# Kernel tuning notes

Hardware: AMD Instinct MI355X
Metric: run time of the kernel (lower is better)

## Reference

```python
import jax, jax.numpy as jnp
import numpy as np

L_LAYERS = 3
N_EGO = 1024
N_EDGE = 49152
M_MODES = 6
HID = 256
N_HEADS = 8
LN_EPS = 1e-5


def _layernorm(x, w, b):
    mu = jnp.mean(x, axis=-1, keepdims=True)
    var = jnp.var(x, axis=-1, keepdims=True)
    return (x - mu) * jax.lax.rsqrt(var + LN_EPS) * w + b


def setup_inputs() -> dict:
    key = jax.random.key(0)
    ks = jax.random.split(key, 16)
    f32 = jnp.float32
    H, Hh, L = HID, HID // 2, L_LAYERS

    def p(k, shape, s=0.02):
        return jax.random.normal(k, shape, f32) * s

    inp = {
        "batch": jnp.sort(jax.random.randint(ks[0], (N_EDGE,), 0, N_EGO)),
        "ego_feature": jax.random.normal(ks[1], (N_EGO, M_MODES, H), f32),
        "edge_feat": jax.random.normal(ks[2], (N_EDGE, M_MODES, Hh), f32),
        "node_feat": jax.random.normal(ks[3], (N_EDGE, M_MODES, Hh), f32),
        # stacked per-layer params
        "Wk": p(ks[4], (L, Hh, H)), "bk": jnp.zeros((L, H), f32),
        "Wq": p(ks[5], (L, H, H)), "bq": jnp.zeros((L, H), f32),
        "Wv1": p(ks[6], (L, Hh, H)), "bv1": jnp.zeros((L, H), f32),
        "Wv2": p(ks[7], (L, Hh, H)), "bv2": jnp.zeros((L, H), f32),
        "ln1_w": jnp.ones((L, H), f32), "ln1_b": jnp.zeros((L, H), f32),
        "ln2_w": jnp.ones((L, H), f32), "ln2_b": jnp.zeros((L, H), f32),
        "W1": p(ks[8], (L, H, H)), "b1": jnp.zeros((L, H), f32),
        "W2": p(ks[9], (L, H, H)), "b2": jnp.zeros((L, H), f32),
        "Wd": p(ks[10], (L, H, H)), "bd": jnp.zeros((L, H), f32),
    }
    return inp


def reference(batch, ego_feature, edge_feat, node_feat,
              Wk, bk, Wq, bq, Wv1, bv1, Wv2, bv2,
              ln1_w, ln1_b, ln2_w, ln2_b, W1, b1, W2, b2, Wd, bd):
    N, M, H = ego_feature.shape
    E = edge_feat.shape[0]
    h = N_HEADS
    dh = H // h
    L = Wk.shape[0]

    ego = ego_feature
    for i in range(L):
        # --- self-attention block (edge gather -> segment softmax -> scatter sum) ---
        xn = _layernorm(ego, ln1_w[i], ln1_b[i])                 # [N,M,H]
        k = (edge_feat @ Wk[i] + bk[i]).reshape(E, M, h, dh)     # [E,M,h,dh]
        q = (xn @ Wq[i] + bq[i]).reshape(N, M, h, dh)            # [N,M,h,dh]
        v = (edge_feat @ Wv1[i] + bv1[i]
             + node_feat @ Wv2[i] + bv2[i]).reshape(E, M, h, dh)
        scores = jnp.sum(k * q[batch], axis=-1)                  # [E,M,h]
        # segment softmax over edges grouped by ego index
        mx = jax.ops.segment_max(scores, batch, num_segments=N)  # [N,M,h]
        e = jnp.exp(scores - mx[batch])
        denom = jax.ops.segment_sum(e, batch, num_segments=N)
        alpha = e / (denom[batch] + 1e-16)                       # [E,M,h]
        agg = jax.ops.segment_sum((v * alpha[..., None]).reshape(E, M, H),
                                  batch, num_segments=N)         # [N,M,H]
        ego = ego + agg
        # --- ff block (note: 'dropout' in the original is actually a Linear) ---
        yn = _layernorm(ego, ln2_w[i], ln2_b[i])
        hmid = jax.nn.relu(yn @ W1[i] + b1[i])
        hmid = hmid @ Wd[i] + bd[i]
        ego = ego + (hmid @ W2[i] + b2[i])
    return ego
```

## Files before the change

### kernel.cpp

```cpp
#include <hip/hip_runtime.h>
#include <hip/hip_bf16.h>

#define L_LAYERS 3
#define N_EGO    1024
#define N_EDGE   49152
#define M_MODES  6
#define HID      256
#define HH       128
#define NH       8
#define DH       32
#define LN_EPS   1e-5f
#define ESS      (M_MODES * 129)
#define TE       8
#define FR       8

using bf16 = __hip_bfloat16;

__device__ __forceinline__ float cvt(float x) { return x; }
__device__ __forceinline__ float cvt(bf16 x)  { return __bfloat162float(x); }
__device__ __forceinline__ float b2f(unsigned s) {
    union { float f; unsigned u; } x; x.u = s << 16; return x.f;
}

template <typename T>
__device__ __forceinline__ float ldv(const void* p, size_t i) {
    return cvt(((const T*)p)[i]);
}

__device__ __forceinline__ float block_sum256(float v, float* buf) {
    int t = threadIdx.x;
    buf[t] = v;
    __syncthreads();
    #pragma unroll
    for (int s = 128; s > 0; s >>= 1) {
        if (t < s) buf[t] += buf[t + s];
        __syncthreads();
    }
    float r = buf[0];
    __syncthreads();
    return r;
}

__global__ void offsets_kernel(const int* __restrict__ batch, int* __restrict__ offs,
                               const void* __restrict__ ln1w, int* __restrict__ flag) {
    int n = blockIdx.x * blockDim.x + threadIdx.x;
    if (n == 0) {
        const unsigned short* u = (const unsigned short*)ln1w;
        flag[0] = (u[0] == 0x3F80 && u[1] == 0x3F80) ? 0 : 1;
    }
    if (n > N_EGO) return;
    int lo = 0, hi = N_EDGE;
    while (lo < hi) {
        int mid = (lo + hi) >> 1;
        if (batch[mid] < n) lo = mid + 1; else hi = mid;
    }
    offs[n] = lo;
}

template <typename T>
__device__ void init_body(const void* src, float* dst) {
    int i = blockIdx.x * 256 + threadIdx.x;
    dst[i] = ldv<T>(src, i);
}
__global__ void init_kernel(const void* __restrict__ src, float* __restrict__ dst,
                            const int* __restrict__ flag) {
    if (flag[0]) init_body<float>(src, dst); else init_body<bf16>(src, dst);
}

template <typename T>
__device__ void wkt_body(const void* Wk, float* WkT) {
    int idx = blockIdx.x * 256 + threadIdx.x;
    int l   = idx / (HH * HID);
    int rem = idx - l * (HH * HID);
    int j   = rem >> 8;
    int cc  = rem & (HID - 1);
    WkT[(size_t)l * HID * HH + (size_t)cc * HH + j] = ldv<T>(Wk, idx);
}
__global__ void wkt_kernel(const void* __restrict__ Wk, float* __restrict__ WkT,
                           const int* __restrict__ flag) {
    if (flag[0]) wkt_body<float>(Wk, WkT); else wkt_body<bf16>(Wk, WkT);
}

template <typename T>
__device__ void prep_body(const float* ego, const float* WkT, const void* bk,
                          const void* Wq, const void* bq, const void* lnw,
                          const void* lnb, int layer,
                          bf16* qk, float* qb) {
    extern __shared__ float sm[];
    float* xn_s = sm;
    float* q_s  = sm + 1536;
    float* sbuf = sm + 3072;
    int n = blockIdx.x, c = threadIdx.x;
    size_t vo = (size_t)layer * HID;

    float lw = ldv<T>(lnw, vo + c), lb = ldv<T>(lnb, vo + c);
    for (int m = 0; m < M_MODES; m++) {
        float x  = ego[((size_t)n * M_MODES + m) * HID + c];
        float mu = block_sum256(x, sbuf) * (1.0f / HID);
        float d  = x - mu;
        float var = block_sum256(d * d, sbuf) * (1.0f / HID);
        xn_s[m * HID + c] = d * rsqrtf(var + LN_EPS) * lw + lb;
    }
    __syncthreads();

    {
        size_t wo = (size_t)layer * HID * HID;
        float acc[M_MODES];
        float bqv = ldv<T>(bq, vo + c);
        #pragma unroll
        for (int m = 0; m < M_MODES; m++) acc[m] = bqv;
        for (int k = 0; k < HID; k++) {
            float w = ldv<T>(Wq, wo + (size_t)k * HID + c);
            #pragma unroll
            for (int m = 0; m < M_MODES; m++) acc[m] += xn_s[m * HID + k] * w;
        }
        #pragma unroll
        for (int m = 0; m < M_MODES; m++) q_s[m * HID + c] = acc[m];
    }
    __syncthreads();

    {
        const float* WT = WkT + (size_t)layer * HID * HH;
        int j = c & (HH - 1), hg = c >> 7;
        #pragma unroll
        for (int hh = 0; hh < NH / 2; hh++) {
            int h = hg * (NH / 2) + hh;
            float a[M_MODES];
            #pragma unroll
            for (int m = 0; m < M_MODES; m++) a[m] = 0.f;
            for (int u = 0; u < DH; u++) {
                float w = WT[(size_t)(h * DH + u) * HH + j];
                #pragma unroll
                for (int m = 0; m < M_MODES; m++)
                    a[m] += q_s[m * HID + h * DH + u] * w;
            }
            #pragma unroll
            for (int m = 0; m < M_MODES; m++)
                qk[((size_t)n * 48 + m * NH + h) * HH + j] = __float2bfloat16(a[m]);
        }
        if (c < M_MODES * NH) {
            int m = c >> 3, h = c & 7;
            float s = 0.f;
            for (int u = 0; u < DH; u++)
                s += ldv<T>(bk, vo + h * DH + u) * q_s[m * HID + h * DH + u];
            qb[n * 48 + c] = s;
        }
    }
}
__global__ void prep_kernel(const float* __restrict__ ego, const float* __restrict__ WkT,
                            const void* __restrict__ bk, const void* __restrict__ Wq,
                            const void* __restrict__ bq, const void* __restrict__ lnw,
                            const void* __restrict__ lnb, int layer,
                            bf16* __restrict__ qk, float* __restrict__ qb,
                            const int* __restrict__ flag) {
    if (flag[0]) prep_body<float>(ego, WkT, bk, Wq, bq, lnw, lnb, layer, qk, qb);
    else         prep_body<bf16 >(ego, WkT, bk, Wq, bq, lnw, lnb, layer, qk, qb);
}

template <typename T>
__device__ void score_body(const void* ef, const bf16* qk, const float* qb,
                           const int* batch, bf16* scores) {
    extern __shared__ float es[];
    int c = threadIdx.x;
    int e0 = blockIdx.x * TE;

    if constexpr (sizeof(T) == 2) {
        const uint4* src = (const uint4*)((const char*)ef + (size_t)e0 * (M_MODES * HH) * 2);
        #pragma unroll
        for (int it = 0; it < 3; it++) {
            int v = it * 256 + c;
            uint4 u = src[v];
            int eo = v / 96, r = v - eo * 96, m = r >> 4, j = (r & 15) * 8;
            float* d = es + eo * ESS + m * 129 + j;
            d[0] = b2f(u.x & 0xffffu); d[1] = b2f(u.x >> 16);
            d[2] = b2f(u.y & 0xffffu); d[3] = b2f(u.y >> 16);
            d[4] = b2f(u.z & 0xffffu); d[5] = b2f(u.z >> 16);
            d[6] = b2f(u.w & 0xffffu); d[7] = b2f(u.w >> 16);
        }
    } else {
        const float4* src = (const float4*)((const char*)ef + (size_t)e0 * (M_MODES * HH) * 4);
        #pragma unroll
        for (int it = 0; it < 6; it++) {
            int v = it * 256 + c;
            float4 u = src[v];
            int eo = v / 192, r = v - eo * 192, m = r >> 5, j = (r & 31) * 4;
            float* d = es + eo * ESS + m * 129 + j;
            d[0] = u.x; d[1] = u.y; d[2] = u.z; d[3] = u.w;
        }
    }
    __syncthreads();

    int g = c & 63, w = c >> 6;
    if (g < M_MODES * NH) {
        #pragma unroll
        for (int sub = 0; sub < TE / 4; sub++) {
            int eo = sub * 4 + w, e = e0 + eo;
            int b = batch[e];
            const uint4* qrow = (const uint4*)(qk + ((size_t)b * 48 + g) * HH);
            const float* ep = es + eo * ESS + (g >> 3) * 129;
            float acc = qb[b * 48 + g];
            #pragma unroll
            for (int v = 0; v < 16; v++) {
                uint4 u = qrow[v];
                const float* e8 = ep + v * 8;
                acc += e8[0] * b2f(u.x & 0xffffu) + e8[1] * b2f(u.x >> 16)
                     + e8[2] * b2f(u.y & 0xffffu) + e8[3] * b2f(u.y >> 16)
                     + e8[4] * b2f(u.z & 0xffffu) + e8[5] * b2f(u.z >> 16)
                     + e8[6] * b2f(u.w & 0xffffu) + e8[7] * b2f(u.w >> 16);
            }
            scores[(size_t)e * 48 + g] = __float2bfloat16(acc);
        }
    }
}
__global__ void score_kernel(const void* __restrict__ ef, const bf16* __restrict__ qk,
                             const float* __restrict__ qb, const int* __restrict__ batch,
                             bf16* __restrict__ scores, const int* __restrict__ flag) {
    if (flag[0]) score_body<float>(ef, qk, qb, batch, scores);
    else         score_body<bf16 >(ef, qk, qb, batch, scores);
}

__global__ void softmax_kernel(bf16* __restrict__ scores, const int* __restrict__ offs) {
    __shared__ float red[4][48];
    int n = blockIdx.x;
    int s0 = offs[n], t1 = offs[n + 1];
    if (s0 >= t1) return;
    int c = threadIdx.x, g = c & 63, w = c >> 6;
    bool act = g < M_MODES * NH;
    float mx = -INFINITY;
    if (act) {
        for (int e = s0 + w; e < t1; e += 4)
            mx = fmaxf(mx, cvt(scores[(size_t)e * 48 + g]));
        red[w][g] = mx;
    }
    __syncthreads();
    if (act) {
        mx = fmaxf(fmaxf(red[0][g], red[1][g]), fmaxf(red[2][g], red[3][g]));
        if (!(mx == mx)) mx = 0.f;
    }
    __syncthreads();
    float den = 0.f;
    if (act) {
        for (int e = s0 + w; e < t1; e += 4) {
            float v = expf(fminf(cvt(scores[(size_t)e * 48 + g]) - mx, 0.f));
            scores[(size_t)e * 48 + g] = __float2bfloat16(v);
            den += v;
        }
        red[w][g] = den;
    }
    __syncthreads();
    if (act) {
        den = red[0][g] + red[1][g] + red[2][g] + red[3][g];
        float inv = 1.0f / (den + 1e-16f);
        for (int e = s0 + w; e < t1; e += 4)
            scores[(size_t)e * 48 + g] =
                __float2bfloat16(cvt(scores[(size_t)e * 48 + g]) * inv);
    }
}

template <typename T>
__device__ void agg_body(const void* ef, const void* nf,
                         const void* Wv1, const void* bv1,
                         const void* Wv2, const void* bv2, int layer,
                         const bf16* alpha, const int* offs, float* ego) {
    extern __shared__ float sm[];
    float* A    = sm;
    float* alf  = sm + 12288;
    float* Ssum = alf + 768;
    int n = blockIdx.x, c = threadIdx.x;
    int s0 = offs[n], t1 = offs[n + 1];
    if (s0 >= t1) return;
    size_t vo = (size_t)layer * HID;
    int part = c >> 7, j = c & (HH - 1);
    const void* src = part ? nf : ef;

    float acc[48];
    #pragma unroll
    for (int i = 0; i < 48; i++) acc[i] = 0.f;
    float sa = 0.f;

    for (int e0 = s0; e0 < t1; e0 += 16) {
        int cnt = t1 - e0; if (cnt > 16) cnt = 16;
        __syncthreads();
        for (int idx = c; idx < cnt * 48; idx += 256)
            alf[idx] = cvt(alpha[(size_t)e0 * 48 + idx]);
        __syncthreads();
        for (int ee = 0; ee < cnt; ee++) {
            size_t ebase = (size_t)(e0 + ee) * (M_MODES * HH) + j;
            const float4* ap = (const float4*)(alf + ee * 48);
            #pragma unroll
            for (int m = 0; m < M_MODES; m++) {
                float val = ldv<T>(src, ebase + m * HH);
                float4 a0 = ap[m * 2 + 0];
                float4 a1 = ap[m * 2 + 1];
                acc[m*8+0] += a0.x * val; acc[m*8+1] += a0.y * val;
                acc[m*8+2] += a0.z * val; acc[m*8+3] += a0.w * val;
                acc[m*8+4] += a1.x * val; acc[m*8+5] += a1.y * val;
                acc[m*8+6] += a1.z * val; acc[m*8+7] += a1.w * val;
            }
        }
        if (c < 48)
            for (int ee = 0; ee < cnt; ee++) sa += alf[ee * 48 + c];
    }
    #pragma unroll
    for (int i = 0; i < 48; i++) A[(part * 48 + i) * HH + j] = acc[i];
    if (c < 48) Ssum[c] = sa;
    __syncthreads();

    size_t wo = (size_t)layer * HH * HID;
    int h = c >> 5;
    float bsum = ldv<T>(bv1, vo + c) + ldv<T>(bv2, vo + c);
    float out[M_MODES];
    #pragma unroll
    for (int m = 0; m < M_MODES; m++) out[m] = bsum * Ssum[m * NH + h];
    for (int jj = 0; jj < HH; jj++) {
        float w1 = ldv<T>(Wv1, wo + (size_t)jj * HID + c);
        float w2 = ldv<T>(Wv2, wo + (size_t)jj * HID + c);
        #pragma unroll
        for (int m = 0; m < M_MODES; m++)
            out[m] += A[(m * NH + h) * HH + jj] * w1
                    + A[(48 + m * NH + h) * HH + jj] * w2;
    }
    #pragma unroll
    for (int m = 0; m < M_MODES; m++)
        ego[((size_t)n * M_MODES + m) * HID + c] += out[m];
}
__global__ void agg_kernel(const void* __restrict__ ef, const void* __restrict__ nf,
                           const void* __restrict__ Wv1, const void* __restrict__ bv1,
                           const void* __restrict__ Wv2, const void* __restrict__ bv2,
                           int layer, const bf16* __restrict__ alpha,
                           const int* __restrict__ offs, float* __restrict__ ego,
                           const int* __restrict__ flag) {
    if (flag[0]) agg_body<float>(ef, nf, Wv1, bv1, Wv2, bv2, layer, alpha, offs, ego);
    else         agg_body<bf16 >(ef, nf, Wv1, bv1, Wv2, bv2, layer, alpha, offs, ego);
}

template <typename T>
__device__ void ffn_body(float* ego, const void* lnw, const void* lnb,
                         const void* W1, const void* b1, const void* Wd, const void* bd,
                         const void* W2, const void* b2, int layer) {
    extern __shared__ float sm[];
    float* xs  = sm;
    float* hs  = sm + 2048;
    float* sb1 = sm + 4096;
    float* sb2 = sm + 4352;
    int r0 = blockIdx.x * FR, c = threadIdx.x;
    size_t wo = (size_t)layer * HID * HID, vo = (size_t)layer * HID;
    float lw = ldv<T>(lnw, vo + c), lb = ldv<T>(lnb, vo + c);
    float x0[FR];
    for (int r = 0; r < FR; r++) {
        float x = ego[(size_t)(r0 + r) * HID + c];
        x0[r] = x;
        sb1[c] = x; sb2[c] = x * x;
        __syncthreads();
        for (int st = 128; st > 0; st >>= 1) {
            if (c < st) { sb1[c] += sb1[c + st]; sb2[c] += sb2[c + st]; }
            __syncthreads();
        }
        float mu  = sb1[0] * (1.0f / HID);
        float var = sb2[0] * (1.0f / HID) - mu * mu;
        __syncthreads();
        xs[r * HID + c] = (x - mu) * rsqrtf(fmaxf(var, 0.f) + LN_EPS) * lw + lb;
    }
    __syncthreads();
    float acc[FR];
    {
        float b = ldv<T>(b1, vo + c);
        #pragma unroll
        for (int r = 0; r < FR; r++) acc[r] = b;
        for (int k = 0; k < HID; k++) {
            float w = ldv<T>(W1, wo + (size_t)k * HID + c);
            #pragma unroll
            for (int r = 0; r < FR; r++) acc[r] += xs[r * HID + k] * w;
        }
        #pragma unroll
        for (int r = 0; r < FR; r++) hs[r * HID + c] = fmaxf(acc[r], 0.f);
    }
    __syncthreads();
    {
        float b = ldv<T>(bd, vo + c);
        #pragma unroll
        for (int r = 0; r < FR; r++) acc[r] = b;
        for (int k = 0; k < HID; k++) {
            float w = ldv<T>(Wd, wo + (size_t)k * HID + c);
            #pragma unroll
            for (int r = 0; r < FR; r++) acc[r] += hs[r * HID + k] * w;
        }
        __syncthreads();
        #pragma unroll
        for (int r = 0; r < FR; r++) xs[r * HID + c] = acc[r];
    }
    __syncthreads();
    {
        float b = ldv<T>(b2, vo + c);
        #pragma unroll
        for (int r = 0; r < FR; r++) acc[r] = b;
        for (int k = 0; k < HID; k++) {
            float w = ldv<T>(W2, wo + (size_t)k * HID + c);
            #pragma unroll
            for (int r = 0; r < FR; r++) acc[r] += xs[r * HID + k] * w;
        }
        #pragma unroll
        for (int r = 0; r < FR; r++)
            ego[(size_t)(r0 + r) * HID + c] = x0[r] + acc[r];
    }
}
__global__ void ffn_kernel(float* __restrict__ ego, const void* __restrict__ lnw,
                           const void* __restrict__ lnb, const void* __restrict__ W1,
                           const void* __restrict__ b1, const void* __restrict__ Wd,
                           const void* __restrict__ bd, const void* __restrict__ W2,
                           const void* __restrict__ b2, int layer,
                           const int* __restrict__ flag) {
    if (flag[0]) ffn_body<float>(ego, lnw, lnb, W1, b1, Wd, bd, W2, b2, layer);
    else         ffn_body<bf16 >(ego, lnw, lnb, W1, b1, Wd, bd, W2, b2, layer);
}

__global__ void out_kernel(const float* __restrict__ src, void* __restrict__ dst,
                           const int* __restrict__ flag) {
    int i = blockIdx.x * 256 + threadIdx.x;
    float v = src[i];
    if (flag[0]) ((float*)dst)[i] = v;
    else         ((bf16*)dst)[i] = __float2bfloat16(v);
}

extern "C" void kernel_launch(void* const* d_in, const int* in_sizes, int n_in,
                              void* d_out, int out_size, void* d_ws, size_t ws_size,
                              hipStream_t stream) {
    const int*  batch = (const int*)d_in[0];
    const void* ego_f = d_in[1];
    const void* edgef = d_in[2];
    const void* nodef = d_in[3];
    const void* Wk  = d_in[4];  const void* bk  = d_in[5];
    const void* Wq  = d_in[6];  const void* bq  = d_in[7];
    const void* Wv1 = d_in[8];  const void* bv1 = d_in[9];
    const void* Wv2 = d_in[10]; const void* bv2 = d_in[11];
    const void* ln1w = d_in[12]; const void* ln1b = d_in[13];
    const void* ln2w = d_in[14]; const void* ln2b = d_in[15];
    const void* W1  = d_in[16]; const void* b1  = d_in[17];
    const void* W2  = d_in[18]; const void* b2  = d_in[19];
    const void* Wd  = d_in[20]; const void* bd  = d_in[21];

    const size_t NMH = (size_t)N_EGO * M_MODES * HID;
    char* ws = (char*)d_ws;
    int*   flag   = (int*)ws;
    int*   offs   = flag + 1;
    float* ego_ws = (float*)(ws + 8192);
    bf16*  scores = (bf16*)(ws + 6299648);
    float* WkT    = (float*)(ws + 11018240);
    bf16*  qk_ws  = (bf16*)(ws + 11411456);
    float* qb_ws  = (float*)(ws + 23994368);

    const int ROWS = N_EGO * M_MODES;

    hipLaunchKernelGGL(offsets_kernel, dim3(5), dim3(256), 0, stream,
                       batch, offs, ln1w, flag);
    hipLaunchKernelGGL(init_kernel, dim3(ROWS), dim3(256), 0, stream,
                       ego_f, ego_ws, flag);
    hipLaunchKernelGGL(wkt_kernel, dim3(L_LAYERS * HH * HID / 256), dim3(256), 0, stream,
                       Wk, WkT, flag);

    const size_t PREP_LDS  = 3328 * 4;
    const size_t SCORE_LDS = (size_t)TE * ESS * 4;
    const size_t AGG_LDS   = (12288 + 768 + 48) * 4;
    const size_t FFN_LDS   = 4608 * 4;

    for (int i = 0; i < L_LAYERS; i++) {
        hipLaunchKernelGGL(prep_kernel, dim3(N_EGO), dim3(256), PREP_LDS, stream,
                           ego_ws, WkT, bk, Wq, bq, ln1w, ln1b, i, qk_ws, qb_ws, flag);
        hipLaunchKernelGGL(score_kernel, dim3(N_EDGE / TE), dim3(256), SCORE_LDS, stream,
                           edgef, qk_ws, qb_ws, batch, scores, flag);
        hipLaunchKernelGGL(softmax_kernel, dim3(N_EGO), dim3(256), 0, stream,
                           scores, offs);
        hipLaunchKernelGGL(agg_kernel, dim3(N_EGO), dim3(256), AGG_LDS, stream,
                           edgef, nodef, Wv1, bv1, Wv2, bv2, i, scores, offs,
                           ego_ws, flag);
        hipLaunchKernelGGL(ffn_kernel, dim3(ROWS / FR), dim3(256), FFN_LDS, stream,
                           ego_ws, ln2w, ln2b, W1, b1, Wd, bd, W2, b2, i, flag);
    }

    hipLaunchKernelGGL(out_kernel, dim3(ROWS), dim3(256), 0, stream,
                       ego_ws, d_out, flag);
}
```

Baseline: 1.321 ms.

## Split aggregation across edge/node parts, vectorize GEMV weight loads, use shuffle reductions

The aggregation kernel now runs on a 2D grid, with one block per ego for edge features and one for node features. Each block stages its feature tile in LDS, uses a padded accumulator layout, and merges results into ego with atomic adds. The prep and FFN matvecs switch from one column per thread to 8 contiguous columns per thread using 16-byte weight loads. LayerNorm reductions use wave shuffles that compute sum and sum-of-squares together, replacing the tree of block barriers. The variance formula changes to E[x^2]-mu^2, and the atomics make the summation order nondeterministic.

```diff
diff --git a/kernel.cpp b/kernel.cpp
--- a/kernel.cpp
+++ b/kernel.cpp
@@ -13,6 +13,7 @@
 #define ESS      (M_MODES * 129)
 #define TE       8
 #define FR       8
+#define AST      129
 
 using bf16 = __hip_bfloat16;
 
@@ -27,18 +28,37 @@
     return cvt(((const T*)p)[i]);
 }
 
-__device__ __forceinline__ float block_sum256(float v, float* buf) {
-    int t = threadIdx.x;
-    buf[t] = v;
-    __syncthreads();
+template <typename T>
+__device__ __forceinline__ void ld8(const void* p, size_t i, float* o);
+template <>
+__device__ __forceinline__ void ld8<bf16>(const void* p, size_t i, float* o) {
+    uint4 u = *(const uint4*)((const bf16*)p + i);
+    o[0] = b2f(u.x & 0xffffu); o[1] = b2f(u.x >> 16);
+    o[2] = b2f(u.y & 0xffffu); o[3] = b2f(u.y >> 16);
+    o[4] = b2f(u.z & 0xffffu); o[5] = b2f(u.z >> 16);
+    o[6] = b2f(u.w & 0xffffu); o[7] = b2f(u.w >> 16);
+}
+template <>
+__device__ __forceinline__ void ld8<float>(const void* p, size_t i, float* o) {
+    const float4* q = (const float4*)((const float*)p + i);
+    float4 a = q[0], b = q[1];
+    o[0] = a.x; o[1] = a.y; o[2] = a.z; o[3] = a.w;
+    o[4] = b.x; o[5] = b.y; o[6] = b.z; o[7] = b.w;
+}
+
+__device__ __forceinline__ void blk_sum2(float a, float b, float* red,
+                                         float* oa, float* ob) {
     #pragma unroll
-    for (int s = 128; s > 0; s >>= 1) {
-        if (t < s) buf[t] += buf[t + s];
-        __syncthreads();
-    }
-    float r = buf[0];
-    __syncthreads();
-    return r;
+    for (int off = 32; off > 0; off >>= 1) {
+        a += __shfl_down(a, off);
+        b += __shfl_down(b, off);
+    }
+    int w = threadIdx.x >> 6;
+    if ((threadIdx.x & 63) == 0) { red[w * 2] = a; red[w * 2 + 1] = b; }
+    __syncthreads();
+    *oa = red[0] + red[2] + red[4] + red[6];
+    *ob = red[1] + red[3] + red[5] + red[7];
+    __syncthreads();
 }
 
 __global__ void offsets_kernel(const int* __restrict__ batch, int* __restrict__ offs,
@@ -89,33 +109,37 @@
     extern __shared__ float sm[];
     float* xn_s = sm;
     float* q_s  = sm + 1536;
-    float* sbuf = sm + 3072;
+    float* red  = sm + 3072;
     int n = blockIdx.x, c = threadIdx.x;
     size_t vo = (size_t)layer * HID;
 
     float lw = ldv<T>(lnw, vo + c), lb = ldv<T>(lnb, vo + c);
     for (int m = 0; m < M_MODES; m++) {
-        float x  = ego[((size_t)n * M_MODES + m) * HID + c];
-        float mu = block_sum256(x, sbuf) * (1.0f / HID);
-        float d  = x - mu;
-        float var = block_sum256(d * d, sbuf) * (1.0f / HID);
-        xn_s[m * HID + c] = d * rsqrtf(var + LN_EPS) * lw + lb;
+        float x = ego[((size_t)n * M_MODES + m) * HID + c];
+        float s1, s2;
+        blk_sum2(x, x * x, red, &s1, &s2);
+        float mu  = s1 * (1.0f / HID);
+        float var = s2 * (1.0f / HID) - mu * mu;
+        xn_s[m * HID + c] = (x - mu) * rsqrtf(fmaxf(var, 0.f) + LN_EPS) * lw + lb;
     }
     __syncthreads();
 
     {
         size_t wo = (size_t)layer * HID * HID;
-        float acc[M_MODES];
-        float bqv = ldv<T>(bq, vo + c);
-        #pragma unroll
-        for (int m = 0; m < M_MODES; m++) acc[m] = bqv;
-        for (int k = 0; k < HID; k++) {
-            float w = ldv<T>(Wq, wo + (size_t)k * HID + c);
-            #pragma unroll
-            for (int m = 0; m < M_MODES; m++) acc[m] += xn_s[m * HID + k] * w;
-        }
-        #pragma unroll
-        for (int m = 0; m < M_MODES; m++) q_s[m * HID + c] = acc[m];
+        int co = (c & 31) * 8, mg = c >> 5;
+        if (mg < M_MODES) {
+            float acc[8], wv[8];
+            ld8<T>(bq, vo + co, acc);
+            #pragma unroll 4
+            for (int k = 0; k < HID; k++) {
+                ld8<T>(Wq, wo + (size_t)k * HID + co, wv);
+                float x = xn_s[mg * HID + k];
+                #pragma unroll
+                for (int i = 0; i < 8; i++) acc[i] += x * wv[i];
+            }
+            #pragma unroll
+            for (int i = 0; i < 8; i++) q_s[mg * HID + co + i] = acc[i];
+        }
     }
     __syncthreads();
 
@@ -262,67 +286,79 @@
                          const void* Wv1, const void* bv1,
                          const void* Wv2, const void* bv2, int layer,
                          const bf16* alpha, const int* offs, float* ego) {
+    constexpr int TILE = (sizeof(T) == 2) ? 16 : 8;
     extern __shared__ float sm[];
     float* A    = sm;
-    float* alf  = sm + 12288;
-    float* Ssum = alf + 768;
-    int n = blockIdx.x, c = threadIdx.x;
+    T*     stage = (T*)sm;
+    float* alf  = sm + 6192;
+    float* Ssum = sm + 6960;
+    int n = blockIdx.x, c = threadIdx.x, part = blockIdx.y;
     int s0 = offs[n], t1 = offs[n + 1];
     if (s0 >= t1) return;
     size_t vo = (size_t)layer * HID;
-    int part = c >> 7, j = c & (HH - 1);
-    const void* src = part ? nf : ef;
-
-    float acc[48];
+    int mh = c >> 7, j = c & (HH - 1);
+    const T* src = (const T*)(part ? nf : ef);
+
+    float acc[24];
     #pragma unroll
-    for (int i = 0; i < 48; i++) acc[i] = 0.f;
+    for (int i = 0; i < 24; i++) acc[i] = 0.f;
     float sa = 0.f;
 
-    for (int e0 = s0; e0 < t1; e0 += 16) {
-        int cnt = t1 - e0; if (cnt > 16) cnt = 16;
+    for (int e0 = s0; e0 < t1; e0 += TILE) {
+        int cnt = t1 - e0; if (cnt > TILE) cnt = TILE;
         __syncthreads();
         for (int idx = c; idx < cnt * 48; idx += 256)
             alf[idx] = cvt(alpha[(size_t)e0 * 48 + idx]);
+        {
+            const uint4* s4 = (const uint4*)(src + (size_t)e0 * (M_MODES * HH));
+            uint4* d4 = (uint4*)stage;
+            int nv = cnt * (M_MODES * HH * (int)sizeof(T) / 16);
+            for (int i = c; i < nv; i += 256) d4[i] = s4[i];
+        }
         __syncthreads();
         for (int ee = 0; ee < cnt; ee++) {
-            size_t ebase = (size_t)(e0 + ee) * (M_MODES * HH) + j;
             const float4* ap = (const float4*)(alf + ee * 48);
             #pragma unroll
-            for (int m = 0; m < M_MODES; m++) {
-                float val = ldv<T>(src, ebase + m * HH);
+            for (int mm = 0; mm < 3; mm++) {
+                int m = mh * 3 + mm;
+                float val = cvt(stage[ee * (M_MODES * HH) + m * HH + j]);
                 float4 a0 = ap[m * 2 + 0];
                 float4 a1 = ap[m * 2 + 1];
-                acc[m*8+0] += a0.x * val; acc[m*8+1] += a0.y * val;
-                acc[m*8+2] += a0.z * val; acc[m*8+3] += a0.w * val;
-                acc[m*8+4] += a1.x * val; acc[m*8+5] += a1.y * val;
-                acc[m*8+6] += a1.z * val; acc[m*8+7] += a1.w * val;
+                acc[mm*8+0] += a0.x * val; acc[mm*8+1] += a0.y * val;
+                acc[mm*8+2] += a0.z * val; acc[mm*8+3] += a0.w * val;
+                acc[mm*8+4] += a1.x * val; acc[mm*8+5] += a1.y * val;
+                acc[mm*8+6] += a1.z * val; acc[mm*8+7] += a1.w * val;
             }
         }
         if (c < 48)
             for (int ee = 0; ee < cnt; ee++) sa += alf[ee * 48 + c];
     }
+    __syncthreads();
     #pragma unroll
-    for (int i = 0; i < 48; i++) A[(part * 48 + i) * HH + j] = acc[i];
+    for (int mm = 0; mm < 3; mm++)
+        #pragma unroll
+        for (int hh = 0; hh < 8; hh++)
+            A[((mh * 3 + mm) * 8 + hh) * AST + j] = acc[mm * 8 + hh];
     if (c < 48) Ssum[c] = sa;
     __syncthreads();
 
     size_t wo = (size_t)layer * HH * HID;
+    const void* Wv = part ? Wv2 : Wv1;
+    const void* bv = part ? bv2 : bv1;
     int h = c >> 5;
-    float bsum = ldv<T>(bv1, vo + c) + ldv<T>(bv2, vo + c);
+    float bb = ldv<T>(bv, vo + c);
     float out[M_MODES];
     #pragma unroll
-    for (int m = 0; m < M_MODES; m++) out[m] = bsum * Ssum[m * NH + h];
+    for (int m = 0; m < M_MODES; m++) out[m] = bb * Ssum[m * NH + h];
     for (int jj = 0; jj < HH; jj++) {
-        float w1 = ldv<T>(Wv1, wo + (size_t)jj * HID + c);
-        float w2 = ldv<T>(Wv2, wo + (size_t)jj * HID + c);
+        float w = ldv<T>(Wv, wo + (size_t)jj * HID + c);
         #pragma unroll
         for (int m = 0; m < M_MODES; m++)
-            out[m] += A[(m * NH + h) * HH + jj] * w1
-                    + A[(48 + m * NH + h) * HH + jj] * w2;
+            out[m] += A[(m * NH + h) * AST + jj] * w;
     }
     #pragma unroll
     for (int m = 0; m < M_MODES; m++)
-        ego[((size_t)n * M_MODES + m) * HID + c] += out[m];
+        atomicAdd(&ego[((size_t)n * M_MODES + m) * HID + c], out[m]);
 }
 __global__ void agg_kernel(const void* __restrict__ ef, const void* __restrict__ nf,
                            const void* __restrict__ Wv1, const void* __restrict__ bv1,
@@ -341,67 +377,63 @@
     extern __shared__ float sm[];
     float* xs  = sm;
     float* hs  = sm + 2048;
-    float* sb1 = sm + 4096;
-    float* sb2 = sm + 4352;
+    float* x0s = sm + 4096;
+    float* red = sm + 6144;
     int r0 = blockIdx.x * FR, c = threadIdx.x;
     size_t wo = (size_t)layer * HID * HID, vo = (size_t)layer * HID;
+
     float lw = ldv<T>(lnw, vo + c), lb = ldv<T>(lnb, vo + c);
-    float x0[FR];
     for (int r = 0; r < FR; r++) {
         float x = ego[(size_t)(r0 + r) * HID + c];
-        x0[r] = x;
-        sb1[c] = x; sb2[c] = x * x;
-        __syncthreads();
-        for (int st = 128; st > 0; st >>= 1) {
-            if (c < st) { sb1[c] += sb1[c + st]; sb2[c] += sb2[c + st]; }
-            __syncthreads();
-        }
-        float mu  = sb1[0] * (1.0f / HID);
-        float var = sb2[0] * (1.0f / HID) - mu * mu;
-        __syncthreads();
+        x0s[r * HID + c] = x;
+        float s1, s2;
+        blk_sum2(x, x * x, red, &s1, &s2);
+        float mu  = s1 * (1.0f / HID);
+        float var = s2 * (1.0f / HID) - mu * mu;
         xs[r * HID + c] = (x - mu) * rsqrtf(fmaxf(var, 0.f) + LN_EPS) * lw + lb;
     }
     __syncthreads();
-    float acc[FR];
+
+    int co = (c & 31) * 8, r = c >> 5;
+    float acc[8], wv[8];
     {
-        float b = ldv<T>(b1, vo + c);
-        #pragma unroll
-        for (int r = 0; r < FR; r++) acc[r] = b;
+        ld8<T>(b1, vo + co, acc);
+        #pragma unroll 4
         for (int k = 0; k < HID; k++) {
-            float w = ldv<T>(W1, wo + (size_t)k * HID + c);
-            #pragma unroll
-            for (int r = 0; r < FR; r++) acc[r] += xs[r * HID + k] * w;
-        }
-        #pragma unroll
-        for (int r = 0; r < FR; r++) hs[r * HID + c] = fmaxf(acc[r], 0.f);
+            ld8<T>(W1, wo + (size_t)k * HID + co, wv);
+            float x = xs[r * HID + k];
+            #pragma unroll
+            for (int i = 0; i < 8; i++) acc[i] += x * wv[i];
+        }
+        #pragma unroll
+        for (int i = 0; i < 8; i++) hs[r * HID + co + i] = fmaxf(acc[i], 0.f);
     }
     __syncthreads();
     {
-        float b = ldv<T>(bd, vo + c);
-        #pragma unroll
-        for (int r = 0; r < FR; r++) acc[r] = b;
+        ld8<T>(bd, vo + co, acc);
+        #pragma unroll 4
         for (int k = 0; k < HID; k++) {
-            float w = ldv<T>(Wd, wo + (size_t)k * HID + c);
-            #pragma unroll
-            for (int r = 0; r < FR; r++) acc[r] += hs[r * HID + k] * w;
-        }
-        __syncthreads();
-        #pragma unroll
-        for (int r = 0; r < FR; r++) xs[r * HID + c] = acc[r];
+            ld8<T>(Wd, wo + (size_t)k * HID + co, wv);
+            float x = hs[r * HID + k];
+            #pragma unroll
+            for (int i = 0; i < 8; i++) acc[i] += x * wv[i];
+        }
+        #pragma unroll
+        for (int i = 0; i < 8; i++) xs[r * HID + co + i] = acc[i];
     }
     __syncthreads();
     {
-        float b = ldv<T>(b2, vo + c);
-        #pragma unroll
-        for (int r = 0; r < FR; r++) acc[r] = b;
+        ld8<T>(b2, vo + co, acc);
+        #pragma unroll 4
         for (int k = 0; k < HID; k++) {
-            float w = ldv<T>(W2, wo + (size_t)k * HID + c);
-            #pragma unroll
-            for (int r = 0; r < FR; r++) acc[r] += xs[r * HID + k] * w;
-        }
-        #pragma unroll
-        for (int r = 0; r < FR; r++)
-            ego[(size_t)(r0 + r) * HID + c] = x0[r] + acc[r];
+            ld8<T>(W2, wo + (size_t)k * HID + co, wv);
+            float x = xs[r * HID + k];
+            #pragma unroll
+            for (int i = 0; i < 8; i++) acc[i] += x * wv[i];
+        }
+        float* eg = ego + (size_t)(r0 + r) * HID + co;
+        #pragma unroll
+        for (int i = 0; i < 8; i++) eg[i] = x0s[r * HID + co + i] + acc[i];
     }
 }
 __global__ void ffn_kernel(float* __restrict__ ego, const void* __restrict__ lnw,
@@ -458,10 +490,10 @@
     hipLaunchKernelGGL(wkt_kernel, dim3(L_LAYERS * HH * HID / 256), dim3(256), 0, stream,
                        Wk, WkT, flag);
 
-    const size_t PREP_LDS  = 3328 * 4;
+    const size_t PREP_LDS  = 3080 * 4;
     const size_t SCORE_LDS = (size_t)TE * ESS * 4;
-    const size_t AGG_LDS   = (12288 + 768 + 48) * 4;
-    const size_t FFN_LDS   = 4608 * 4;
+    const size_t AGG_LDS   = 7008 * 4;
+    const size_t FFN_LDS   = 6152 * 4;
 
     for (int i = 0; i < L_LAYERS; i++) {
         hipLaunchKernelGGL(prep_kernel, dim3(N_EGO), dim3(256), PREP_LDS, stream,
@@ -470,7 +502,7 @@
                            edgef, qk_ws, qb_ws, batch, scores, flag);
         hipLaunchKernelGGL(softmax_kernel, dim3(N_EGO), dim3(256), 0, stream,
                            scores, offs);
-        hipLaunchKernelGGL(agg_kernel, dim3(N_EGO), dim3(256), AGG_LDS, stream,
+        hipLaunchKernelGGL(agg_kernel, dim3(N_EGO, 2), dim3(256), AGG_LDS, stream,
                            edgef, nodef, Wv1, bv1, Wv2, bv2, i, scores, offs,
                            ego_ws, flag);
         hipLaunchKernelGGL(ffn_kernel, dim3(ROWS / FR), dim3(256), FFN_LDS, stream,
```

After: 1.485 ms. 1.12x slower.
